# Kernel tuning notes

Hardware: AMD Instinct MI355X
Metric: run time of the kernel (lower is better)

Reference implementation:

```python
import jax, jax.numpy as jnp
import numpy as np

R_MIN = 0.01
R_MAX = 0.6
H = 32            # polar radial bins (after pooling)
W = 64            # polar angular bins (after pooling)
UP_R = 10         # radial upsampling factor
UP_T = 10         # angular upsampling factor
ATT_ALPHA = 5.0
B, C, IMG = 64, 3, 224


def _conv(x, w, b):
    # NCHW valid conv, stride 1 (matches nn.Conv2d default padding=0)
    y = jax.lax.conv_general_dilated(x, w, (1, 1), 'VALID',
                                     dimension_numbers=('NCHW', 'OIHW', 'NCHW'))
    return y + b[None, :, None, None]


def _maxpool2(x):
    return jax.lax.reduce_window(x, -jnp.inf, jax.lax.max,
                                 (1, 1, 2, 2), (1, 1, 2, 2), 'VALID')


def _grid_sample_border(x, grid):
    # F.grid_sample, bilinear, padding_mode='border', align_corners=False
    Bn, Cn, Hi, Wi = x.shape
    ix = ((grid[..., 0] + 1.0) * Wi - 1.0) * 0.5   # x-coord -> width index
    iy = ((grid[..., 1] + 1.0) * Hi - 1.0) * 0.5   # y-coord -> height index
    x0f = jnp.floor(ix)
    y0f = jnp.floor(iy)
    wx = (ix - x0f)[..., None]
    wy = (iy - y0f)[..., None]
    x0 = jnp.clip(x0f.astype(jnp.int32), 0, Wi - 1)
    x1 = jnp.clip(x0f.astype(jnp.int32) + 1, 0, Wi - 1)
    y0 = jnp.clip(y0f.astype(jnp.int32), 0, Hi - 1)
    y1 = jnp.clip(y0f.astype(jnp.int32) + 1, 0, Hi - 1)
    bidx = jnp.arange(Bn)[:, None, None]
    v00 = x[bidx, :, y0, x0]   # [B,Hg,Wg,C]
    v01 = x[bidx, :, y0, x1]
    v10 = x[bidx, :, y1, x0]
    v11 = x[bidx, :, y1, x1]
    out = (v00 * (1 - wx) * (1 - wy) + v01 * wx * (1 - wy)
           + v10 * (1 - wx) * wy + v11 * wx * wy)
    return jnp.transpose(out, (0, 3, 1, 2))  # [B,C,Hg,Wg]


def setup_inputs() -> dict:
    key = jax.random.key(0)
    ks = jax.random.split(key, 10)
    x = jax.random.normal(ks[0], (B, C, IMG, IMG), dtype=jnp.float32)
    l_t_prev = jax.random.uniform(ks[1], (B, 2), dtype=jnp.float32)
    conv1_w = jax.random.normal(ks[2], (6, C, 5, 5), dtype=jnp.float32) * 0.1
    conv1_b = jnp.zeros((6,), jnp.float32)
    conv2_w = jax.random.normal(ks[3], (16, 6, 5, 5), dtype=jnp.float32) * 0.1
    conv2_b = jnp.zeros((16,), jnp.float32)
    fc1_w = jax.random.normal(ks[4], (8, 16), dtype=jnp.float32) * 0.1
    fc1_b = jnp.zeros((8,), jnp.float32)
    fc2_w = jax.random.normal(ks[5], (2, 8), dtype=jnp.float32) * 0.1
    fc2_b = jnp.zeros((2,), jnp.float32)
    return dict(x=x, l_t_prev=l_t_prev, conv1_w=conv1_w, conv1_b=conv1_b,
                conv2_w=conv2_w, conv2_b=conv2_b, fc1_w=fc1_w, fc1_b=fc1_b,
                fc2_w=fc2_w, fc2_b=fc2_b)


def reference(x, l_t_prev, conv1_w, conv1_b, conv2_w, conv2_b,
              fc1_w, fc1_b, fc2_w, fc2_b):
    # --- attention branch: conv -> maxpool -> conv -> GAP -> fc -> sigmoid ---
    h = _conv(x, conv1_w, conv1_b)
    h = _maxpool2(h)
    h = _conv(h, conv2_w, conv2_b)
    feat = h.mean(axis=(2, 3))                     # AdaptiveAvgPool2d(1), [B,16]
    h = jax.nn.relu(feat @ fc1_w.T + fc1_b)
    weight = jax.nn.sigmoid(h @ fc2_w.T + fc2_b) * ATT_ALPHA   # [B,2]
    # --- per-batch log-polar grid ---
    Hg, Wg = H * UP_R, W * UP_T
    angle = 2.0 * jnp.pi * jnp.arange(Wg, dtype=jnp.float32) / Wg
    unit = jnp.stack([jnp.sin(angle), jnp.cos(angle)], axis=-1)   # [Wg,2]
    start = jnp.log(R_MIN * weight[:, 0])
    stop = jnp.log(R_MAX * weight[:, 1])
    t = jnp.arange(Hg, dtype=jnp.float32) / (Hg - 1)
    radii = jnp.exp(start[:, None] + (stop - start)[:, None] * t[None])  # [B,Hg]
    grid = radii[:, :, None, None] * unit[None, None]     # [B,Hg,Wg,2]
    grid = grid + l_t_prev[:, None, None, :]
    # --- irregular bilinear sampling + box filter ---
    sampled = _grid_sample_border(x, grid)                 # [B,C,Hg,Wg]
    Bn, Cn = sampled.shape[:2]
    pooled = sampled.reshape(Bn, Cn, H, UP_R, W, UP_T).mean(axis=(3, 5))
    return pooled, weight
```

## Files before the change

kernel.cpp:

```cpp
#include <hip/hip_runtime.h>
#include <math.h>

#define Bn    64
#define Cn    3
#define IMG   224
#define PLANE (IMG*IMG)
#define C1    6
#define P1    110
#define P2    106
#define NVALID (P2*P2)
#define Hh    32
#define Ww    64
#define UPR   10
#define UPT   10
#define Hg    (Hh*UPR)
#define Wg    (Ww*UPT)
#define POOLED_SIZE (Bn*Cn*Hh*Ww)
#define RPB   4
#define NCHUNK ((P1 + RPB - 1) / RPB)
#define PSTRIDE 152

typedef unsigned short u16;

#define PART_FLOATS ((size_t)Bn * NCHUNK * PSTRIDE)
#define X4B_U16     ((size_t)Bn * PLANE * 4)
#define WS_NEEDED   ((PART_FLOATS + Bn * 2) * 4 + X4B_U16 * 2)

__device__ __forceinline__ u16 f2bf(float f) {
    union { unsigned int u; float f; } c; c.f = f;
    unsigned int r = c.u + 0x7fffu + ((c.u >> 16) & 1u);
    return (u16)(r >> 16);
}
__device__ __forceinline__ float bf2f(u16 v) {
    union { unsigned int u; float f; } c; c.u = ((unsigned int)v) << 16;
    return c.f;
}

__global__ __launch_bounds__(256) void k1_fused(
    const float* __restrict__ x,
    const float* __restrict__ w1,
    const float* __restrict__ b1,
    float* __restrict__ partial,
    u16* __restrict__ x4b,
    int do_pack)
{
    __shared__ __attribute__((aligned(16))) float xs[3][12][224];
    __shared__ float psum[RPB][PSTRIDE];

    const int b    = blockIdx.y;
    const int chunk = blockIdx.x;
    const int y0   = chunk * RPB;
    const int tid  = threadIdx.x;
    const int wid  = tid >> 6;
    const int lane = tid & 63;

    const float* xb = x + (size_t)b * (Cn * PLANE);
    const int gybase = 2 * y0;

    for (int i = tid; i < 3 * 12 * 56; i += 256) {
        const int ic  = i / (12 * 56);
        const int rem = i - ic * (12 * 56);
        const int r   = rem / 56;
        const int c4  = rem - r * 56;
        const int gy  = gybase + r;
        if (gy < IMG)
            *(float4*)(&xs[ic][r][c4 * 4]) =
                *(const float4*)(xb + ic * PLANE + gy * IMG + c4 * 4);
    }
    __syncthreads();

    if (do_pack) {
        u16* ob = x4b + (size_t)b * PLANE * 4;
        for (int i = tid; i < 8 * IMG; i += 256) {
            const int r   = i / IMG;
            const int col = i - r * IMG;
            const int gy  = gybase + r;
            ushort4 v;
            v.x = f2bf(xs[0][r][col]);
            v.y = f2bf(xs[1][r][col]);
            v.z = f2bf(xs[2][r][col]);
            v.w = 0;
            *(ushort4*)(ob + ((size_t)gy * IMG + col) * 4) = v;
        }
    }

    const int y = y0 + wid;
    const bool rowvalid = (y < P1);
    const bool active = (lane < 55) && rowvalid;

    float pp0[C1], pp1[C1];
    if (active) {
        float acc[C1][8];
        #pragma unroll
        for (int oc = 0; oc < C1; ++oc) {
            const float bv = b1[oc];
            #pragma unroll
            for (int j = 0; j < 8; ++j) acc[oc][j] = bv;
        }

        #pragma unroll
        for (int ic = 0; ic < 3; ++ic) {
            float rTop[8], rBot[8];
            {
                const float* rp = &xs[ic][2 * wid][4 * lane];
                const float4 a = *(const float4*)rp;
                const float4 c = *(const float4*)(rp + 4);
                rTop[0]=a.x; rTop[1]=a.y; rTop[2]=a.z; rTop[3]=a.w;
                rTop[4]=c.x; rTop[5]=c.y; rTop[6]=c.z; rTop[7]=c.w;
            }
            {
                const float* rp = &xs[ic][2 * wid + 1][4 * lane];
                const float4 a = *(const float4*)rp;
                const float4 c = *(const float4*)(rp + 4);
                rBot[0]=a.x; rBot[1]=a.y; rBot[2]=a.z; rBot[3]=a.w;
                rBot[4]=c.x; rBot[5]=c.y; rBot[6]=c.z; rBot[7]=c.w;
            }
            #pragma unroll
            for (int ky = 0; ky < 5; ++ky) {
                #pragma unroll
                for (int oc = 0; oc < C1; ++oc) {
                    const float* wrow = w1 + ((oc * 3 + ic) * 25 + ky * 5);
                    #pragma unroll
                    for (int kx = 0; kx < 5; ++kx) {
                        const float wv = wrow[kx];
                        acc[oc][0] += rTop[kx    ] * wv;
                        acc[oc][1] += rTop[kx + 1] * wv;
                        acc[oc][2] += rTop[kx + 2] * wv;
                        acc[oc][3] += rTop[kx + 3] * wv;
                        acc[oc][4] += rBot[kx    ] * wv;
                        acc[oc][5] += rBot[kx + 1] * wv;
                        acc[oc][6] += rBot[kx + 2] * wv;
                        acc[oc][7] += rBot[kx + 3] * wv;
                    }
                }
                if (ky < 4) {
                    #pragma unroll
                    for (int j = 0; j < 8; ++j) rTop[j] = rBot[j];
                    const float* rp = &xs[ic][2 * wid + ky + 2][4 * lane];
                    const float4 a = *(const float4*)rp;
                    const float4 c = *(const float4*)(rp + 4);
                    rBot[0]=a.x; rBot[1]=a.y; rBot[2]=a.z; rBot[3]=a.w;
                    rBot[4]=c.x; rBot[5]=c.y; rBot[6]=c.z; rBot[7]=c.w;
                }
            }
        }

        #pragma unroll
        for (int oc = 0; oc < C1; ++oc) {
            pp0[oc] = fmaxf(fmaxf(acc[oc][0], acc[oc][1]),
                            fmaxf(acc[oc][4], acc[oc][5]));
            pp1[oc] = fmaxf(fmaxf(acc[oc][2], acc[oc][3]),
                            fmaxf(acc[oc][6], acc[oc][7]));
        }
    } else {
        #pragma unroll
        for (int oc = 0; oc < C1; ++oc) { pp0[oc] = 0.0f; pp1[oc] = 0.0f; }
    }

    #pragma unroll
    for (int oc = 0; oc < C1; ++oc) {
        float s = pp0[oc] + pp1[oc];
        #pragma unroll
        for (int off = 32; off > 0; off >>= 1) s += __shfl_xor(s, off, 64);
        const float c0   = __shfl(pp0[oc], 0, 64);
        const float c1   = __shfl(pp1[oc], 0, 64);
        const float c2   = __shfl(pp0[oc], 1, 64);
        const float c3   = __shfl(pp1[oc], 1, 64);
        const float c106 = __shfl(pp0[oc], 53, 64);
        const float c107 = __shfl(pp1[oc], 53, 64);
        const float c108 = __shfl(pp0[oc], 54, 64);
        const float c109 = __shfl(pp1[oc], 54, 64);
        const float w0v = s - (c106 + c107 + c108 + c109);
        const float w1v = s - c0 - (c107 + c108 + c109);
        const float w2v = s - (c0 + c1) - (c108 + c109);
        const float w3v = s - (c0 + c1 + c2) - c109;
        const float w4v = s - (c0 + c1 + c2 + c3);
        if (lane < 25) {
            const int ky = lane / 5;
            const int kx = lane % 5;
            float wv = w0v;
            wv = (kx == 1) ? w1v : wv;
            wv = (kx == 2) ? w2v : wv;
            wv = (kx == 3) ? w3v : wv;
            wv = (kx == 4) ? w4v : wv;
            const bool valid = rowvalid && ((unsigned)(y - ky) <= 105u);
            psum[wid][oc * 25 + lane] = valid ? wv : 0.0f;
        }
    }
    __syncthreads();

    if (tid < 150) {
        const float v = psum[0][tid] + psum[1][tid] + psum[2][tid] + psum[3][tid];
        partial[((size_t)b * NCHUNK + chunk) * PSTRIDE + tid] = v;
    }
}

__global__ __launch_bounds__(256) void k2_head(
    const float* __restrict__ partial, const float* __restrict__ w2,
    const float* __restrict__ b2, const float* __restrict__ fc1w,
    const float* __restrict__ fc1b, const float* __restrict__ fc2w,
    const float* __restrict__ fc2b, float* __restrict__ wt_ws,
    float* __restrict__ out)
{
    const int b = blockIdx.x;
    const int tid = threadIdx.x;
    __shared__ float wsb[150];
    __shared__ float sfeat[16];
    __shared__ float sh[8];

    if (tid < 150) {
        const float* p = partial + (size_t)b * NCHUNK * PSTRIDE + tid;
        float s = 0.0f;
        #pragma unroll
        for (int c = 0; c < NCHUNK; ++c) s += p[c * PSTRIDE];
        wsb[tid] = s;
    }
    __syncthreads();
    if (tid < 16) {
        float s = 0.0f;
        for (int j = 0; j < 150; ++j) s += w2[tid * 150 + j] * wsb[j];
        sfeat[tid] = b2[tid] + s * (1.0f / (float)NVALID);
    }
    __syncthreads();
    if (tid < 8) {
        float s = fc1b[tid];
        #pragma unroll
        for (int j = 0; j < 16; ++j) s += fc1w[tid * 16 + j] * sfeat[j];
        sh[tid] = fmaxf(s, 0.0f);
    }
    __syncthreads();
    if (tid < 2) {
        float s = fc2b[tid];
        #pragma unroll
        for (int j = 0; j < 8; ++j) s += fc2w[tid * 8 + j] * sh[j];
        float sig = (s >= 0.0f) ? (1.0f / (1.0f + expf(-s)))
                                : (expf(s) / (1.0f + expf(s)));
        const float wgt = 5.0f * sig;
        wt_ws[b * 2 + tid] = wgt;
        out[POOLED_SIZE + b * 2 + tid] = wgt;
    }
}

__device__ __forceinline__ void sample_coords(
    float gxn, float gyn, int& x0, int& y0, float& wx, float& wy)
{
    float ix = ((gxn + 1.0f) * (float)IMG - 1.0f) * 0.5f;
    float iy = ((gyn + 1.0f) * (float)IMG - 1.0f) * 0.5f;
    ix = fminf(fmaxf(ix, 0.0f), (float)(IMG - 1));
    iy = fminf(fmaxf(iy, 0.0f), (float)(IMG - 1));
    x0 = (int)ix; if (x0 > IMG - 2) x0 = IMG - 2;
    y0 = (int)iy; if (y0 > IMG - 2) y0 = IMG - 2;
    wx = ix - (float)x0;
    wy = iy - (float)y0;
}

__global__ __launch_bounds__(640) void k3_sample_pool_bf16(
    const u16* __restrict__ x4b,
    const float* __restrict__ ltp,
    const float* __restrict__ wt,
    float* __restrict__ out)
{
    __shared__ float part[3 * Wg];

    const int L = blockIdx.x;
    const int q = L >> 3;
    const int h = q & 31;
    const int b = (L & 7) + 8 * (q >> 5);
    const int tid = threadIdx.x;

    const float w0 = wt[b * 2 + 0];
    const float w1 = wt[b * 2 + 1];
    const float l0 = ltp[b * 2 + 0];
    const float l1 = ltp[b * 2 + 1];
    const float start = logf(0.01f * w0);
    const float stop  = logf(0.6f  * w1);
    const float dr = stop - start;

    const float angle = 6.283185307179586f * (float)tid / (float)Wg;
    const float sn = sinf(angle);
    const float cs = cosf(angle);

    const u16* xb4 = x4b + (size_t)b * PLANE * 4;

    const float ratio = expf(dr * (1.0f / (float)(Hg - 1)));
    float r = expf(start + dr * ((float)(h * UPR) / (float)(Hg - 1)));

    float acc0 = 0.0f, acc1 = 0.0f, acc2 = 0.0f;
    #pragma unroll
    for (int i = 0; i < UPR; ++i) {
        int x0, y0; float wx, wy;
        sample_coords(r * sn + l0, r * cs + l1, x0, y0, wx, wy);
        r *= ratio;

        const u16* base = xb4 + ((size_t)(y0 * IMG + x0)) * 4;
        const ushort4 a00 = *(const ushort4*)(base);
        const ushort4 a01 = *(const ushort4*)(base + 4);
        const ushort4 a10 = *(const ushort4*)(base + IMG * 4);
        const ushort4 a11 = *(const ushort4*)(base + IMG * 4 + 4);

        const float wx0 = 1.0f - wx, wy0 = 1.0f - wy;
        const float w00 = wx0 * wy0, w01 = wx * wy0;
        const float w10 = wx0 * wy,  w11 = wx * wy;

        acc0 += w00*bf2f(a00.x) + w01*bf2f(a01.x) + w10*bf2f(a10.x) + w11*bf2f(a11.x);
        acc1 += w00*bf2f(a00.y) + w01*bf2f(a01.y) + w10*bf2f(a10.y) + w11*bf2f(a11.y);
        acc2 += w00*bf2f(a00.z) + w01*bf2f(a01.z) + w10*bf2f(a10.z) + w11*bf2f(a11.z);
    }
    part[0 * Wg + tid] = acc0;
    part[1 * Wg + tid] = acc1;
    part[2 * Wg + tid] = acc2;
    __syncthreads();

    if (tid < Cn * Ww) {
        const int c = tid / Ww;
        const int w = tid % Ww;
        const float* p = part + c * Wg + w * UPT;
        float s = 0.0f;
        #pragma unroll
        for (int j = 0; j < UPT; ++j) s += p[j];
        out[(((size_t)b * Cn + c) * Hh + h) * Ww + w] = s * (1.0f / (UPR * UPT));
    }
}

__global__ __launch_bounds__(640) void k3_sample_pool_nchw(
    const float* __restrict__ x, const float* __restrict__ ltp,
    const float* __restrict__ wt, float* __restrict__ out)
{
    __shared__ float part[3 * Wg];
    const int L = blockIdx.x;
    const int q = L >> 3;
    const int h = q & 31;
    const int b = (L & 7) + 8 * (q >> 5);
    const int tid = threadIdx.x;

    const float w0 = wt[b * 2 + 0];
    const float w1 = wt[b * 2 + 1];
    const float l0 = ltp[b * 2 + 0];
    const float l1 = ltp[b * 2 + 1];
    const float start = logf(0.01f * w0);
    const float stop  = logf(0.6f  * w1);
    const float dr = stop - start;
    const float angle = 6.283185307179586f * (float)tid / (float)Wg;
    const float sn = sinf(angle);
    const float cs = cosf(angle);
    const float* xb = x + (size_t)b * Cn * PLANE;

    const float ratio = expf(dr * (1.0f / (float)(Hg - 1)));
    float r = expf(start + dr * ((float)(h * UPR) / (float)(Hg - 1)));

    float acc0 = 0.0f, acc1 = 0.0f, acc2 = 0.0f;
    #pragma unroll
    for (int i = 0; i < UPR; ++i) {
        int x0, y0; float wx, wy;
        sample_coords(r * sn + l0, r * cs + l1, x0, y0, wx, wy);
        r *= ratio;
        const float wx0 = 1.0f - wx, wy0 = 1.0f - wy;
        const float w00 = wx0 * wy0, w01 = wx * wy0;
        const float w10 = wx0 * wy,  w11 = wx * wy;
        const int o00 = y0 * IMG + x0;
        acc0 += w00*xb[o00] + w01*xb[o00+1] + w10*xb[o00+IMG] + w11*xb[o00+IMG+1];
        const float* x1p = xb + PLANE;
        acc1 += w00*x1p[o00] + w01*x1p[o00+1] + w10*x1p[o00+IMG] + w11*x1p[o00+IMG+1];
        const float* x2p = xb + 2 * PLANE;
        acc2 += w00*x2p[o00] + w01*x2p[o00+1] + w10*x2p[o00+IMG] + w11*x2p[o00+IMG+1];
    }
    part[0 * Wg + tid] = acc0;
    part[1 * Wg + tid] = acc1;
    part[2 * Wg + tid] = acc2;
    __syncthreads();

    if (tid < Cn * Ww) {
        const int c = tid / Ww;
        const int w = tid % Ww;
        const float* p = part + c * Wg + w * UPT;
        float s = 0.0f;
        #pragma unroll
        for (int j = 0; j < UPT; ++j) s += p[j];
        out[(((size_t)b * Cn + c) * Hh + h) * Ww + w] = s * (1.0f / (UPR * UPT));
    }
}

extern "C" void kernel_launch(void* const* d_in, const int* in_sizes, int n_in,
                              void* d_out, int out_size, void* d_ws, size_t ws_size,
                              hipStream_t stream) {
    const float* x       = (const float*)d_in[0];
    const float* ltp     = (const float*)d_in[1];
    const float* conv1_w = (const float*)d_in[2];
    const float* conv1_b = (const float*)d_in[3];
    const float* conv2_w = (const float*)d_in[4];
    const float* conv2_b = (const float*)d_in[5];
    const float* fc1_w   = (const float*)d_in[6];
    const float* fc1_b   = (const float*)d_in[7];
    const float* fc2_w   = (const float*)d_in[8];
    const float* fc2_b   = (const float*)d_in[9];
    float* out = (float*)d_out;

    const int do_pack = (ws_size >= WS_NEEDED) ? 1 : 0;

    float* part_ws = (float*)d_ws;
    float* wt_ws   = part_ws + PART_FLOATS;
    u16*   x4b     = (u16*)(wt_ws + Bn * 2);

    k1_fused<<<dim3(NCHUNK, Bn), dim3(256), 0, stream>>>(
        x, conv1_w, conv1_b, part_ws, x4b, do_pack);
    k2_head<<<dim3(Bn), dim3(256), 0, stream>>>(part_ws, conv2_w, conv2_b,
                                                fc1_w, fc1_b, fc2_w, fc2_b,
                                                wt_ws, out);
    if (do_pack)
        k3_sample_pool_bf16<<<dim3(Hh * Bn), dim3(Wg), 0, stream>>>(x4b, ltp, wt_ws, out);
    else
        k3_sample_pool_nchw<<<dim3(Hh * Bn), dim3(Wg), 0, stream>>>(x, ltp, wt_ws, out);
}
```

Baseline: 184.4 us.

## Use packed float2 FMAs in conv1 and process two row chunks per block

The conv1+maxpool kernel now accumulates pairs of adjacent outputs in 2-wide float vectors, so the compiler can emit packed fp32 FMA instructions, roughly halving the FMA instruction count. Input rows are loaded as overlapping pairs, and the top/bottom buffers alternate instead of being copied each step. Each block also loops over two consecutive row chunks, halving the grid size. This trades fewer blocks, and so less latency hiding, plus extra register pressure for denser arithmetic and less per-block launch overhead.

```diff
diff --git a/kernel.cpp b/kernel.cpp
--- a/kernel.cpp
+++ b/kernel.cpp
@@ -21,6 +21,7 @@
 #define PSTRIDE 152
 
 typedef unsigned short u16;
+typedef float v2f __attribute__((ext_vector_type(2)));
 
 #define PART_FLOATS ((size_t)Bn * NCHUNK * PSTRIDE)
 #define X4B_U16     ((size_t)Bn * PLANE * 4)
@@ -34,6 +35,18 @@
 __device__ __forceinline__ float bf2f(u16 v) {
     union { unsigned int u; float f; } c; c.u = ((unsigned int)v) << 16;
     return c.f;
+}
+
+__device__ __forceinline__ void load_pairs(v2f* P, const float* rp) {
+    const float4 a = *(const float4*)rp;
+    const float4 c = *(const float4*)(rp + 4);
+    P[0] = (v2f){a.x, a.y};
+    P[1] = (v2f){a.y, a.z};
+    P[2] = (v2f){a.z, a.w};
+    P[3] = (v2f){a.w, c.x};
+    P[4] = (v2f){c.x, c.y};
+    P[5] = (v2f){c.y, c.z};
+    P[6] = (v2f){c.z, c.w};
 }
 
 __global__ __launch_bounds__(256) void k1_fused(
@@ -48,150 +61,135 @@
     __shared__ float psum[RPB][PSTRIDE];
 
     const int b    = blockIdx.y;
-    const int chunk = blockIdx.x;
-    const int y0   = chunk * RPB;
     const int tid  = threadIdx.x;
     const int wid  = tid >> 6;
     const int lane = tid & 63;
 
     const float* xb = x + (size_t)b * (Cn * PLANE);
-    const int gybase = 2 * y0;
-
-    for (int i = tid; i < 3 * 12 * 56; i += 256) {
-        const int ic  = i / (12 * 56);
-        const int rem = i - ic * (12 * 56);
-        const int r   = rem / 56;
-        const int c4  = rem - r * 56;
-        const int gy  = gybase + r;
-        if (gy < IMG)
-            *(float4*)(&xs[ic][r][c4 * 4]) =
-                *(const float4*)(xb + ic * PLANE + gy * IMG + c4 * 4);
-    }
-    __syncthreads();
-
-    if (do_pack) {
-        u16* ob = x4b + (size_t)b * PLANE * 4;
-        for (int i = tid; i < 8 * IMG; i += 256) {
-            const int r   = i / IMG;
-            const int col = i - r * IMG;
+
+    for (int half = 0; half < 2; ++half) {
+        const int chunk = 2 * blockIdx.x + half;
+        const int y0 = chunk * RPB;
+        const int gybase = 2 * y0;
+
+        for (int i = tid; i < 3 * 12 * 56; i += 256) {
+            const int ic  = i / (12 * 56);
+            const int rem = i - ic * (12 * 56);
+            const int r   = rem / 56;
+            const int c4  = rem - r * 56;
             const int gy  = gybase + r;
-            ushort4 v;
-            v.x = f2bf(xs[0][r][col]);
-            v.y = f2bf(xs[1][r][col]);
-            v.z = f2bf(xs[2][r][col]);
-            v.w = 0;
-            *(ushort4*)(ob + ((size_t)gy * IMG + col) * 4) = v;
+            if (gy < IMG)
+                *(float4*)(&xs[ic][r][c4 * 4]) =
+                    *(const float4*)(xb + ic * PLANE + gy * IMG + c4 * 4);
         }
-    }
-
-    const int y = y0 + wid;
-    const bool rowvalid = (y < P1);
-    const bool active = (lane < 55) && rowvalid;
-
-    float pp0[C1], pp1[C1];
-    if (active) {
-        float acc[C1][8];
-        #pragma unroll
-        for (int oc = 0; oc < C1; ++oc) {
-            const float bv = b1[oc];
+        __syncthreads();
+
+        if (do_pack) {
+            u16* ob = x4b + (size_t)b * PLANE * 4;
+            for (int i = tid; i < 8 * IMG; i += 256) {
+                const int r   = i / IMG;
+                const int col = i - r * IMG;
+                const int gy  = gybase + r;
+                ushort4 v;
+                v.x = f2bf(xs[0][r][col]);
+                v.y = f2bf(xs[1][r][col]);
+                v.z = f2bf(xs[2][r][col]);
+                v.w = 0;
+                *(ushort4*)(ob + ((size_t)gy * IMG + col) * 4) = v;
+            }
+        }
+
+        const int y = y0 + wid;
+        const bool rowvalid = (y < P1);
+        const bool active = (lane < 55) && rowvalid;
+
+        float pp0[C1], pp1[C1];
+        if (active) {
+            v2f accT01[C1], accT23[C1], accB01[C1], accB23[C1];
             #pragma unroll
-            for (int j = 0; j < 8; ++j) acc[oc][j] = bv;
-        }
-
-        #pragma unroll
-        for (int ic = 0; ic < 3; ++ic) {
-            float rTop[8], rBot[8];
-            {
-                const float* rp = &xs[ic][2 * wid][4 * lane];
-                const float4 a = *(const float4*)rp;
-                const float4 c = *(const float4*)(rp + 4);
-                rTop[0]=a.x; rTop[1]=a.y; rTop[2]=a.z; rTop[3]=a.w;
-                rTop[4]=c.x; rTop[5]=c.y; rTop[6]=c.z; rTop[7]=c.w;
+            for (int oc = 0; oc < C1; ++oc) {
+                const float bv = b1[oc];
+                const v2f bvv = (v2f){bv, bv};
+                accT01[oc] = bvv; accT23[oc] = bvv;
+                accB01[oc] = bvv; accB23[oc] = bvv;
             }
-            {
-                const float* rp = &xs[ic][2 * wid + 1][4 * lane];
-                const float4 a = *(const float4*)rp;
-                const float4 c = *(const float4*)(rp + 4);
-                rBot[0]=a.x; rBot[1]=a.y; rBot[2]=a.z; rBot[3]=a.w;
-                rBot[4]=c.x; rBot[5]=c.y; rBot[6]=c.z; rBot[7]=c.w;
-            }
+
             #pragma unroll
-            for (int ky = 0; ky < 5; ++ky) {
+            for (int ic = 0; ic < 3; ++ic) {
+                v2f Pa[7], Pb[7];
+                load_pairs(Pa, &xs[ic][2 * wid][4 * lane]);
+                load_pairs(Pb, &xs[ic][2 * wid + 1][4 * lane]);
                 #pragma unroll
-                for (int oc = 0; oc < C1; ++oc) {
-                    const float* wrow = w1 + ((oc * 3 + ic) * 25 + ky * 5);
+                for (int ky = 0; ky < 5; ++ky) {
+                    const v2f* Pt = (ky & 1) ? Pb : Pa;
+                    const v2f* Po = (ky & 1) ? Pa : Pb;
                     #pragma unroll
-                    for (int kx = 0; kx < 5; ++kx) {
-                        const float wv = wrow[kx];
-                        acc[oc][0] += rTop[kx    ] * wv;
-                        acc[oc][1] += rTop[kx + 1] * wv;
-                        acc[oc][2] += rTop[kx + 2] * wv;
-                        acc[oc][3] += rTop[kx + 3] * wv;
-                        acc[oc][4] += rBot[kx    ] * wv;
-                        acc[oc][5] += rBot[kx + 1] * wv;
-                        acc[oc][6] += rBot[kx + 2] * wv;
-                        acc[oc][7] += rBot[kx + 3] * wv;
+                    for (int oc = 0; oc < C1; ++oc) {
+                        const float* wrow = w1 + ((oc * 3 + ic) * 25 + ky * 5);
+                        #pragma unroll
+                        for (int kx = 0; kx < 5; ++kx) {
+                            const float wv = wrow[kx];
+                            const v2f wvv = (v2f){wv, wv};
+                            accT01[oc] += Pt[kx]     * wvv;
+                            accT23[oc] += Pt[kx + 2] * wvv;
+                            accB01[oc] += Po[kx]     * wvv;
+                            accB23[oc] += Po[kx + 2] * wvv;
+                        }
                     }
-                }
-                if (ky < 4) {
-                    #pragma unroll
-                    for (int j = 0; j < 8; ++j) rTop[j] = rBot[j];
-                    const float* rp = &xs[ic][2 * wid + ky + 2][4 * lane];
-                    const float4 a = *(const float4*)rp;
-                    const float4 c = *(const float4*)(rp + 4);
-                    rBot[0]=a.x; rBot[1]=a.y; rBot[2]=a.z; rBot[3]=a.w;
-                    rBot[4]=c.x; rBot[5]=c.y; rBot[6]=c.z; rBot[7]=c.w;
+                    if (ky < 4)
+                        load_pairs((ky & 1) ? Pb : Pa,
+                                   &xs[ic][2 * wid + ky + 2][4 * lane]);
                 }
             }
+
+            #pragma unroll
+            for (int oc = 0; oc < C1; ++oc) {
+                pp0[oc] = fmaxf(fmaxf(accT01[oc].x, accT01[oc].y),
+                                fmaxf(accB01[oc].x, accB01[oc].y));
+                pp1[oc] = fmaxf(fmaxf(accT23[oc].x, accT23[oc].y),
+                                fmaxf(accB23[oc].x, accB23[oc].y));
+            }
+        } else {
+            #pragma unroll
+            for (int oc = 0; oc < C1; ++oc) { pp0[oc] = 0.0f; pp1[oc] = 0.0f; }
         }
 
         #pragma unroll
         for (int oc = 0; oc < C1; ++oc) {
-            pp0[oc] = fmaxf(fmaxf(acc[oc][0], acc[oc][1]),
-                            fmaxf(acc[oc][4], acc[oc][5]));
-            pp1[oc] = fmaxf(fmaxf(acc[oc][2], acc[oc][3]),
-                            fmaxf(acc[oc][6], acc[oc][7]));
+            float s = pp0[oc] + pp1[oc];
+            #pragma unroll
+            for (int off = 32; off > 0; off >>= 1) s += __shfl_xor(s, off, 64);
+            const float c0   = __shfl(pp0[oc], 0, 64);
+            const float c1   = __shfl(pp1[oc], 0, 64);
+            const float c2   = __shfl(pp0[oc], 1, 64);
+            const float c3   = __shfl(pp1[oc], 1, 64);
+            const float c106 = __shfl(pp0[oc], 53, 64);
+            const float c107 = __shfl(pp1[oc], 53, 64);
+            const float c108 = __shfl(pp0[oc], 54, 64);
+            const float c109 = __shfl(pp1[oc], 54, 64);
+            const float w0v = s - (c106 + c107 + c108 + c109);
+            const float w1v = s - c0 - (c107 + c108 + c109);
+            const float w2v = s - (c0 + c1) - (c108 + c109);
+            const float w3v = s - (c0 + c1 + c2) - c109;
+            const float w4v = s - (c0 + c1 + c2 + c3);
+            if (lane < 25) {
+                const int ky = lane / 5;
+                const int kx = lane % 5;
+                float wv = w0v;
+                wv = (kx == 1) ? w1v : wv;
+                wv = (kx == 2) ? w2v : wv;
+                wv = (kx == 3) ? w3v : wv;
+                wv = (kx == 4) ? w4v : wv;
+                const bool valid = rowvalid && ((unsigned)(y - ky) <= 105u);
+                psum[wid][oc * 25 + lane] = valid ? wv : 0.0f;
+            }
         }
-    } else {
-        #pragma unroll
-        for (int oc = 0; oc < C1; ++oc) { pp0[oc] = 0.0f; pp1[oc] = 0.0f; }
-    }
-
-    #pragma unroll
-    for (int oc = 0; oc < C1; ++oc) {
-        float s = pp0[oc] + pp1[oc];
-        #pragma unroll
-        for (int off = 32; off > 0; off >>= 1) s += __shfl_xor(s, off, 64);
-        const float c0   = __shfl(pp0[oc], 0, 64);
-        const float c1   = __shfl(pp1[oc], 0, 64);
-        const float c2   = __shfl(pp0[oc], 1, 64);
-        const float c3   = __shfl(pp1[oc], 1, 64);
-        const float c106 = __shfl(pp0[oc], 53, 64);
-        const float c107 = __shfl(pp1[oc], 53, 64);
-        const float c108 = __shfl(pp0[oc], 54, 64);
-        const float c109 = __shfl(pp1[oc], 54, 64);
-        const float w0v = s - (c106 + c107 + c108 + c109);
-        const float w1v = s - c0 - (c107 + c108 + c109);
-        const float w2v = s - (c0 + c1) - (c108 + c109);
-        const float w3v = s - (c0 + c1 + c2) - c109;
-        const float w4v = s - (c0 + c1 + c2 + c3);
-        if (lane < 25) {
-            const int ky = lane / 5;
-            const int kx = lane % 5;
-            float wv = w0v;
-            wv = (kx == 1) ? w1v : wv;
-            wv = (kx == 2) ? w2v : wv;
-            wv = (kx == 3) ? w3v : wv;
-            wv = (kx == 4) ? w4v : wv;
-            const bool valid = rowvalid && ((unsigned)(y - ky) <= 105u);
-            psum[wid][oc * 25 + lane] = valid ? wv : 0.0f;
+        __syncthreads();
+
+        if (tid < 150) {
+            const float v = psum[0][tid] + psum[1][tid] + psum[2][tid] + psum[3][tid];
+            partial[((size_t)b * NCHUNK + chunk) * PSTRIDE + tid] = v;
         }
-    }
-    __syncthreads();
-
-    if (tid < 150) {
-        const float v = psum[0][tid] + psum[1][tid] + psum[2][tid] + psum[3][tid];
-        partial[((size_t)b * NCHUNK + chunk) * PSTRIDE + tid] = v;
     }
 }
 
@@ -401,7 +399,7 @@
     float* wt_ws   = part_ws + PART_FLOATS;
     u16*   x4b     = (u16*)(wt_ws + Bn * 2);
 
-    k1_fused<<<dim3(NCHUNK, Bn), dim3(256), 0, stream>>>(
+    k1_fused<<<dim3(NCHUNK / 2, Bn), dim3(256), 0, stream>>>(
         x, conv1_w, conv1_b, part_ws, x4b, do_pack);
     k2_head<<<dim3(Bn), dim3(256), 0, stream>>>(part_ws, conv2_w, conv2_b,
                                                 fc1_w, fc1_b, fc2_w, fc2_b,
```

Result: faster. 176.3 us (-4.4%).
